# Optimization experiments

Hardware: AMD Instinct MI355X
Metric: run time of the kernel (lower is better)

## Reference

```python
import jax, jax.numpy as jnp
import numpy as np

B, C, D, DE, NH = 4, 4, 96, 96, 3
NS, HIN, TOTAL_Z, PZ = 12, 128, 64, 32
WZ = WH = WW = 4
N_WIN_TOK = WZ * WH * WW  # 64 tokens per 3D window


def _rel_index():
    # standard Swin-3D relative position index, (N, N) into a (7*7*7, NH) table
    c = np.stack(np.meshgrid(np.arange(WZ), np.arange(WH), np.arange(WW), indexing='ij')).reshape(3, -1)
    r = (c[:, :, None] - c[:, None, :]).transpose(1, 2, 0)
    r += np.array([WZ - 1, WH - 1, WW - 1])
    r[:, :, 0] *= (2 * WH - 1) * (2 * WW - 1)
    r[:, :, 1] *= (2 * WW - 1)
    return jnp.asarray(r.sum(-1))

REL_IDX = _rel_index()


def layernorm(x, g, b, eps=1e-5):
    m = x.mean(-1, keepdims=True)
    v = x.var(-1, keepdims=True)
    return (x - m) * jax.lax.rsqrt(v + eps) * g + b


def groupnorm(x, g, b, groups=8, eps=1e-5):
    Bb, Cc, Z, H, W = x.shape
    xr = x.reshape(Bb, groups, Cc // groups, Z, H, W)
    m = xr.mean((2, 3, 4, 5), keepdims=True)
    v = xr.var((2, 3, 4, 5), keepdims=True)
    xr = (xr - m) * jax.lax.rsqrt(v + eps)
    return xr.reshape(Bb, Cc, Z, H, W) * g[None, :, None, None, None] + b[None, :, None, None, None]


def conv3d(x, w, b):
    y = jax.lax.conv_general_dilated(x, w, (1, 1, 1), 'SAME', dimension_numbers=('NCDHW', 'OIDHW', 'NCDHW'))
    return y + b[None, :, None, None, None]


def z_interp(x, pos, out_z):
    """Linear interp along z. x:(B,C,S,H,W), pos:(S,) sorted float positions.
    Matches the torch loop: clamp below first / above last, weight=0.5 on ties."""
    S = x.shape[2]
    zq = jnp.arange(out_z, dtype=jnp.float32)
    right = jnp.searchsorted(pos, zq, side='left')  # first i with pos[i] >= z
    left = jnp.clip(right - 1, 0, S - 1)
    rc = jnp.clip(right, 0, S - 1)
    lp, rp = pos[left], pos[rc]
    d = rp - lp
    w = jnp.where(d > 0, (zq - lp) / jnp.where(d > 0, d, 1.0), 0.5)
    w = w[None, None, :, None, None]
    return (1.0 - w) * x[:, :, left] + w * x[:, :, rc]


def reference(sparse_obs, encoder_feat, pe_w, pe_b, pe_g, pe_beta, enc_w, enc_b, ln_g, ln_b,
              qkv_w, qkv_b, attn_w, attn_b, rpb, ref_w1, ref_b1, gn1_g, gn1_b,
              ref_w2, ref_b2, gn2_g, gn2_b, rec_w, rec_b, sparse_indices):
    Bb, Cc, Sz, H, W = sparse_obs.shape
    pos = sparse_indices.astype(jnp.float32)
    # --- skip connection: z-interp baseline at full resolution ---
    baseline = z_interp(sparse_obs, pos, TOTAL_Z)  # (B,C,64,128,128)
    # --- sparse patch embed: conv (1,4,4) stride (1,4,4) + LN ---
    xr = sparse_obs.reshape(Bb, Cc, Sz, H // 4, 4, W // 4, 4)
    f = jnp.einsum('bczhpwq,dcpq->bdzhw', xr, pe_w) + pe_b[None, :, None, None, None]
    f = layernorm(f.transpose(0, 2, 3, 4, 1), pe_g, pe_beta).transpose(0, 4, 1, 2, 3)
    # position-aware z interpolation into patch space (patch_size_z = 2)
    f = z_interp(f, pos / 2.0, PZ)  # (B,D,32,32,32)
    # --- encoder 1x1x1 projection + fuse ---
    enc = jnp.einsum('bczhw,dc->bdzhw', encoder_feat, enc_w) + enc_b[None, :, None, None, None]
    f = f + enc
    # --- 3D window attention with relative position bias (pre-norm, residual) ---
    nz = PZ // WZ
    x = f.transpose(0, 2, 3, 4, 1)  # (B,Z,H,W,D)
    xw = x.reshape(Bb, nz, WZ, nz, WH, nz, WW, D).transpose(0, 1, 3, 5, 2, 4, 6, 7).reshape(-1, N_WIN_TOK, D)
    sc = xw
    xn = layernorm(xw, ln_g, ln_b)
    dh = D // NH
    qkv = (xn @ qkv_w.T + qkv_b).reshape(-1, N_WIN_TOK, 3, NH, dh).transpose(2, 0, 3, 1, 4)
    q, k, v = qkv[0], qkv[1], qkv[2]  # (nWin*B, NH, N, dh)
    att = jnp.einsum('whnd,whmd->whnm', q * (dh ** -0.5), k)
    att = att + rpb[REL_IDX].transpose(2, 0, 1)[None]  # (.., NH, N, N)
    att = jax.nn.softmax(att, axis=-1)
    o = jnp.einsum('whnm,whmd->whnd', att, v).transpose(0, 2, 1, 3).reshape(-1, N_WIN_TOK, D)
    xw = sc + (o @ attn_w.T + attn_b)
    x = xw.reshape(Bb, nz, nz, nz, WZ, WH, WW, D).transpose(0, 1, 4, 2, 5, 3, 6, 7).reshape(Bb, PZ, PZ, PZ, D)
    f = x.transpose(0, 4, 1, 2, 3)
    f = jax.nn.gelu(groupnorm(conv3d(f, ref_w1, ref_b1), gn1_g, gn1_b), approximate=False)
    f = jax.nn.gelu(groupnorm(conv3d(f, ref_w2, ref_b2), gn2_g, gn2_b), approximate=False)
    # --- patch recovery: ConvTranspose3d kernel=stride=(2,4,4) as einsum+reshape ---
    delta = jnp.einsum('bizhw,iodef->bozdhewf', f, rec_w).reshape(Bb, Cc, PZ * 2, PZ * 4, PZ * 4)
    delta = delta + rec_b[None, :, None, None, None]
    return baseline + delta


def setup_inputs():
    key = jax.random.key(0)
    ks = jax.random.split(key, 16)
    n = lambda i, shape: jax.random.normal(ks[i], shape, dtype=jnp.float32) * 0.02
    return {
        'sparse_obs': jax.random.normal(ks[0], (B, C, NS, HIN, HIN), dtype=jnp.float32),
        'encoder_feat': jax.random.normal(ks[1], (B, DE, PZ, PZ, PZ), dtype=jnp.float32),
        'pe_w': n(2, (D, C, 4, 4)), 'pe_b': jnp.zeros((D,)), 'pe_g': jnp.ones((D,)), 'pe_beta': jnp.zeros((D,)),
        'enc_w': n(3, (D, DE)), 'enc_b': jnp.zeros((D,)),
        'ln_g': jnp.ones((D,)), 'ln_b': jnp.zeros((D,)),
        'qkv_w': n(4, (3 * D, D)), 'qkv_b': jnp.zeros((3 * D,)),
        'attn_w': n(5, (D, D)), 'attn_b': jnp.zeros((D,)),
        'rpb': n(6, ((2 * WZ - 1) * (2 * WH - 1) * (2 * WW - 1), NH)),
        'ref_w1': n(7, (D, D, 3, 3, 3)), 'ref_b1': jnp.zeros((D,)), 'gn1_g': jnp.ones((D,)), 'gn1_b': jnp.zeros((D,)),
        'ref_w2': n(8, (D, D, 3, 3, 3)), 'ref_b2': jnp.zeros((D,)), 'gn2_g': jnp.ones((D,)), 'gn2_b': jnp.zeros((D,)),
        'rec_w': n(9, (D, C, 2, 4, 4)), 'rec_b': jnp.zeros((C,)),
        'sparse_indices': jnp.asarray(np.round(np.linspace(0, 63, 12)).astype(np.int64)),
    }
```

## Files before the change

kernel.cpp:

```cpp
#include <hip/hip_runtime.h>
#include <math.h>

typedef __attribute__((ext_vector_type(8))) short short8v;
typedef __attribute__((ext_vector_type(4))) float float4v;

__device__ inline unsigned short f2bf(float f) {
  unsigned u = __float_as_uint(f);
  return (unsigned short)((u + 0x7fff + ((u >> 16) & 1)) >> 16);
}
__device__ inline unsigned pk2(float a, float b) {
  return (unsigned)f2bf(a) | ((unsigned)f2bf(b) << 16);
}
__device__ inline float bfl(unsigned u) { return __uint_as_float(u << 16); }
__device__ inline float bfh(unsigned u) { return __uint_as_float(u & 0xffff0000u); }
__device__ inline float bfs(short s) { return __uint_as_float(((unsigned)(unsigned short)s) << 16); }

__global__ __launch_bounds__(96) void k_tables(const int* __restrict__ sidx, int* __restrict__ T) {
  __shared__ float pos[12];
  int t = threadIdx.x;
  if (t < 12) pos[t] = (float)sidx[t];
  __syncthreads();
  if (t < 64) {
    float zq = (float)t;
    int r = 0;
    while (r < 12 && pos[r] < zq) r++;
    int l = r - 1; if (l < 0) l = 0; if (l > 11) l = 11;
    int rc = r; if (rc > 11) rc = 11;
    float lp = pos[l], rp = pos[rc], d = rp - lp;
    float w = d > 0.f ? (zq - lp) / d : 0.5f;
    T[t] = l; T[64 + t] = rc; ((float*)T)[128 + t] = w;
  } else {
    int zq = t - 64;
    float zqf = (float)zq;
    int r = 0;
    while (r < 12 && pos[r] * 0.5f < zqf) r++;
    int l = r - 1; if (l < 0) l = 0; if (l > 11) l = 11;
    int rc = r; if (rc > 11) rc = 11;
    float lp = pos[l] * 0.5f, rp = pos[rc] * 0.5f, d = rp - lp;
    float w = d > 0.f ? (zqf - lp) / d : 0.5f;
    T[192 + zq] = l; T[224 + zq] = rc; ((float*)T)[256 + zq] = w;
  }
}

__global__ __launch_bounds__(256) void k_wcv(const float* __restrict__ w, short* __restrict__ Wt) {
  int id = blockIdx.x * 256 + threadIdx.x;
  if (id >= 248832) return;
  float v = w[id];
  int o = id / 2592; int rem = id % 2592; int i = rem / 27; int tap = rem % 27;
  Wt[(tap * 96 + o) * 96 + i] = (short)f2bf(v);
}

__global__ __launch_bounds__(256) void k_cvt(const float* __restrict__ src, short* __restrict__ dst, int n) {
  int id = blockIdx.x * 256 + threadIdx.x;
  if (id < n) dst[id] = (short)f2bf(src[id]);
}

__global__ __launch_bounds__(256) void k_wrt(const float* __restrict__ src, short* __restrict__ dst) {
  int id = blockIdx.x * 256 + threadIdx.x;
  if (id >= 12288) return;
  int i = id >> 7, j = id & 127;
  dst[j * 96 + i] = (short)f2bf(src[id]);
}

__global__ __launch_bounds__(256) void k_bias(const float* __restrict__ rpb, float* __restrict__ Bt) {
  int id = blockIdx.x * 256 + threadIdx.x;
  if (id >= 12288) return;
  int head = id >> 12, rem = id & 4095, n = rem >> 6, m = rem & 63;
  int dz = (n >> 4) - (m >> 4), dh = ((n >> 2) & 3) - ((m >> 2) & 3), dw = (n & 3) - (m & 3);
  Bt[id] = rpb[((dz + 3) * 49 + (dh + 3) * 7 + (dw + 3)) * 3 + head];
}

__global__ __launch_bounds__(256) void k_pe(const float* __restrict__ sp, const short* __restrict__ Wpe,
    const float* __restrict__ pb, const float* __restrict__ pg, const float* __restrict__ pbeta,
    float* __restrict__ f1) {
  int x = blockIdx.x;
  int b = x / 384, z = (x / 32) % 12, h = x % 32;
  __shared__ short sB[32][72];
  __shared__ float sF[32][97];
  __shared__ float sM[32], sR[32];
  int tid = threadIdx.x;
  for (int id = tid; id < 2048; id += 256) {
    int c = id >> 9, p = (id >> 7) & 3, col = id & 127;
    float v = sp[(((b * 4 + c) * 12 + z) * 128 + h * 4 + p) * 128 + col];
    sB[col >> 2][c * 16 + p * 4 + (col & 3)] = (short)f2bf(v);
  }
  __syncthreads();
  int w = tid >> 6, l = tid & 63, lo = l & 15, ig = l >> 4;
  int nt = w & 1, mbase = (w >> 1) * 3;
  short8v bfrag[2];
  #pragma unroll
  for (int kc = 0; kc < 2; kc++)
    bfrag[kc] = *(const short8v*)&sB[nt * 16 + lo][kc * 32 + ig * 8];
  #pragma unroll
  for (int mi = 0; mi < 3; mi++) {
    int m = mbase + mi;
    float4v acc = (float4v){0.f, 0.f, 0.f, 0.f};
    #pragma unroll
    for (int kc = 0; kc < 2; kc++) {
      short8v a = *(const short8v*)(Wpe + (size_t)(m * 16 + lo) * 64 + kc * 32 + ig * 8);
      acc = __builtin_amdgcn_mfma_f32_16x16x32_bf16(a, bfrag[kc], acc, 0, 0, 0);
    }
    int wcoord = nt * 16 + lo;
    #pragma unroll
    for (int r = 0; r < 4; r++) {
      int d = m * 16 + ig * 4 + r;
      sF[wcoord][d] = acc[r] + pb[d];
    }
  }
  __syncthreads();
  if (tid < 32) {
    int wv = tid;
    float s = 0.f, ss = 0.f;
    for (int d = 0; d < 96; d++) { float v = sF[wv][d]; s += v; ss += v * v; }
    float m = s * (1.f / 96.f);
    float var = ss * (1.f / 96.f) - m * m;
    sM[wv] = m; sR[wv] = rsqrtf(var + 1e-5f);
  }
  __syncthreads();
  for (int id = tid; id < 3072; id += 256) {
    int d = id >> 5, wv = id & 31;
    float v = (sF[wv][d] - sM[wv]) * sR[wv] * pg[d] + pbeta[d];
    f1[(((b * 96 + d) * 12 + z) * 32 + h) * 32 + wv] = v;
  }
}

__global__ __launch_bounds__(256) void k_ie(const float* __restrict__ f1, const float* __restrict__ ef,
    const short* __restrict__ Wenc, const float* __restrict__ eb, const int* __restrict__ T,
    unsigned* __restrict__ Xg) {
  int x = blockIdx.x;
  int b = x >> 9, chunk = x & 511;
  int v0 = chunk * 64;
  int z = v0 >> 10, rp = v0 & 1023;
  int zl = T[192 + z], zr = T[224 + z];
  float wt = ((const float*)T)[256 + z];
  __shared__ short sEb[64][104];
  int tid = threadIdx.x;
  for (int id = tid; id < 6144; id += 256) {
    int c = id >> 6, vs = id & 63;
    sEb[vs][c] = (short)f2bf(ef[(size_t)(b * 96 + c) * 32768 + v0 + vs]);
  }
  __syncthreads();
  int w = tid >> 6, l = tid & 63, lo = l & 15, ig = l >> 4;
  int vcol = w * 16 + lo;
  short8v bfrag[3];
  #pragma unroll
  for (int kc = 0; kc < 3; kc++)
    bfrag[kc] = *(const short8v*)&sEb[vcol][kc * 32 + ig * 8];
  float4v acc[6];
  #pragma unroll
  for (int m = 0; m < 6; m++) {
    acc[m] = (float4v){0.f, 0.f, 0.f, 0.f};
    #pragma unroll
    for (int kc = 0; kc < 3; kc++) {
      short8v a = *(const short8v*)(Wenc + (size_t)(m * 16 + lo) * 96 + kc * 32 + ig * 8);
      acc[m] = __builtin_amdgcn_mfma_f32_16x16x32_bf16(a, bfrag[kc], acc[m], 0, 0, 0);
    }
  }
  int zb = z >> 2, tz = z & 3;
  int h0 = (chunk & 15) * 2;
  int h = h0 + (vcol >> 5), wc = vcol & 31;
  int win = ((b * 8 + zb) * 8 + (h >> 2)) * 8 + (wc >> 2);
  int t = tz * 16 + (h & 3) * 4 + (wc & 3);
  size_t xbase = (size_t)(win * 64 + t) * 48;
  float wl = 1.f - wt;
  #pragma unroll
  for (int m = 0; m < 6; m++) {
    #pragma unroll
    for (int rr = 0; rr < 2; rr++) {
      int d0 = m * 16 + ig * 4 + rr * 2;
      const float* p1a = f1 + ((size_t)(b * 96 + d0) * 12 + zl) * 1024 + rp + vcol;
      const float* p2a = f1 + ((size_t)(b * 96 + d0) * 12 + zr) * 1024 + rp + vcol;
      const float* p1b = f1 + ((size_t)(b * 96 + d0 + 1) * 12 + zl) * 1024 + rp + vcol;
      const float* p2b = f1 + ((size_t)(b * 96 + d0 + 1) * 12 + zr) * 1024 + rp + vcol;
      float va = acc[m][rr * 2] + eb[d0] + wl * p1a[0] + wt * p2a[0];
      float vb = acc[m][rr * 2 + 1] + eb[d0 + 1] + wl * p1b[0] + wt * p2b[0];
      Xg[xbase + m * 8 + ig * 2 + rr] = pk2(va, vb);
    }
  }
}

__global__ __launch_bounds__(512) void k_qkv(const unsigned* __restrict__ Xg, const short* __restrict__ Wq,
    const float* __restrict__ qb, const float* __restrict__ lg, const float* __restrict__ lb,
    short* __restrict__ Qg, short* __restrict__ Kg, short* __restrict__ Vg) {
  int win = blockIdx.x;
  __shared__ short sX[64][104];
  __shared__ short sVt[96][72];
  __shared__ float sM[64], sRr[64];
  int tid = threadIdx.x;
  for (int id = tid; id < 3072; id += 512) {
    int row = id / 48, c2 = id % 48;
    *(unsigned*)&sX[row][c2 * 2] = Xg[(size_t)(win * 64 + row) * 48 + c2];
  }
  __syncthreads();
  {
    int token = tid >> 3, j = tid & 7;
    float s = 0.f, ss = 0.f;
    #pragma unroll
    for (int i = 0; i < 12; i++) {
      float v = bfs(sX[token][j * 12 + i]);
      s += v; ss += v * v;
    }
    s += __shfl_xor(s, 1); ss += __shfl_xor(ss, 1);
    s += __shfl_xor(s, 2); ss += __shfl_xor(ss, 2);
    s += __shfl_xor(s, 4); ss += __shfl_xor(ss, 4);
    if (j == 0) {
      float m = s * (1.f / 96.f);
      sM[token] = m;
      sRr[token] = rsqrtf(ss * (1.f / 96.f) - m * m + 1e-5f);
    }
  }
  __syncthreads();
  for (int id = tid; id < 3072; id += 512) {
    int row = id / 48, c2 = id % 48;
    unsigned u = *(unsigned*)&sX[row][c2 * 2];
    float m = sM[row], r = sRr[row];
    float v0 = (bfl(u) - m) * r * lg[2 * c2] + lb[2 * c2];
    float v1 = (bfh(u) - m) * r * lg[2 * c2 + 1] + lb[2 * c2 + 1];
    *(unsigned*)&sX[row][c2 * 2] = pk2(v0, v1);
  }
  __syncthreads();
  int w = tid >> 6, l = tid & 63, lo = l & 15, ig = l >> 4;
  int mt2 = w >> 1, nh = w & 1;
  short8v a[3];
  #pragma unroll
  for (int kc = 0; kc < 3; kc++)
    a[kc] = *(const short8v*)&sX[mt2 * 16 + lo][kc * 32 + ig * 8];
  for (int nt = nh * 9; nt < nh * 9 + 9; nt++) {
    float4v acc = (float4v){0.f, 0.f, 0.f, 0.f};
    #pragma unroll
    for (int kc = 0; kc < 3; kc++) {
      short8v bfr = *(const short8v*)(Wq + (size_t)(nt * 16 + lo) * 96 + kc * 32 + ig * 8);
      acc = __builtin_amdgcn_mfma_f32_16x16x32_bf16(a[kc], bfr, acc, 0, 0, 0);
    }
    int out = nt * 16 + lo;
    float bias = qb[out];
    if (nt < 6) {
      int head = out >> 5, c = out & 31;
      #pragma unroll
      for (int r = 0; r < 4; r++)
        Qg[((size_t)(win * 3 + head) * 64 + mt2 * 16 + ig * 4 + r) * 32 + c] =
            (short)f2bf((acc[r] + bias) * 0.17677669529663687f);
    } else if (nt < 12) {
      int o2 = out - 96, head = o2 >> 5, c = o2 & 31;
      #pragma unroll
      for (int r = 0; r < 4; r++)
        Kg[((size_t)(win * 3 + head) * 64 + mt2 * 16 + ig * 4 + r) * 32 + c] = (short)f2bf(acc[r] + bias);
    } else {
      int o2 = out - 192;
      #pragma unroll
      for (int r = 0; r < 4; r++)
        sVt[o2][mt2 * 16 + ig * 4 + r] = (short)f2bf(acc[r] + bias);
    }
  }
  __syncthreads();
  for (int id = tid; id < 768; id += 512) {
    int row = id >> 3, ch = id & 7;
    short8v v = *(short8v*)&sVt[row][ch * 8];
    *(short8v*)(Vg + ((size_t)(win * 3 + (row >> 5)) * 32 + (row & 31)) * 64 + ch * 8) = v;
  }
}

__global__ __launch_bounds__(256) void k_att2(const short* __restrict__ Qg, const short* __restrict__ Kg,
    const short* __restrict__ Vg, const float* __restrict__ Bt, short* __restrict__ Og) {
  __shared__ short Pl[4][64][72];
  int tid = threadIdx.x;
  int w = tid >> 6, l = tid & 63, lo = l & 15, ig = l >> 4;
  int gwh = blockIdx.x * 4 + w;
  int head = gwh % 3, win = gwh / 3;
  short8v q[4], k[4];
  #pragma unroll
  for (int mt = 0; mt < 4; mt++)
    q[mt] = *(const short8v*)(Qg + ((size_t)gwh * 64 + mt * 16 + lo) * 32 + ig * 8);
  #pragma unroll
  for (int nt = 0; nt < 4; nt++)
    k[nt] = *(const short8v*)(Kg + ((size_t)gwh * 64 + nt * 16 + lo) * 32 + ig * 8);
  float4v s[4][4];
  #pragma unroll
  for (int mt = 0; mt < 4; mt++)
    #pragma unroll
    for (int nt = 0; nt < 4; nt++)
      s[mt][nt] = __builtin_amdgcn_mfma_f32_16x16x32_bf16(q[mt], k[nt], (float4v){0.f, 0.f, 0.f, 0.f}, 0, 0, 0);
  const float* bt = Bt + head * 4096;
  #pragma unroll
  for (int mt = 0; mt < 4; mt++) {
    #pragma unroll
    for (int r = 0; r < 4; r++) {
      int tok = mt * 16 + ig * 4 + r;
      float v[4];
      float mx = -1e30f;
      #pragma unroll
      for (int nt = 0; nt < 4; nt++) {
        v[nt] = s[mt][nt][r] + bt[tok * 64 + nt * 16 + lo];
        mx = fmaxf(mx, v[nt]);
      }
      mx = fmaxf(mx, __shfl_xor(mx, 1));
      mx = fmaxf(mx, __shfl_xor(mx, 2));
      mx = fmaxf(mx, __shfl_xor(mx, 4));
      mx = fmaxf(mx, __shfl_xor(mx, 8));
      float sm = 0.f;
      #pragma unroll
      for (int nt = 0; nt < 4; nt++) { v[nt] = __expf(v[nt] - mx); sm += v[nt]; }
      sm += __shfl_xor(sm, 1);
      sm += __shfl_xor(sm, 2);
      sm += __shfl_xor(sm, 4);
      sm += __shfl_xor(sm, 8);
      float inv = 1.f / sm;
      #pragma unroll
      for (int nt = 0; nt < 4; nt++)
        Pl[w][tok][nt * 16 + lo] = (short)f2bf(v[nt] * inv);
    }
  }
  short8v pa[4][2], vb[2][2];
  #pragma unroll
  for (int mt = 0; mt < 4; mt++)
    #pragma unroll
    for (int kc = 0; kc < 2; kc++)
      pa[mt][kc] = *(const short8v*)&Pl[w][mt * 16 + lo][kc * 32 + ig * 8];
  #pragma unroll
  for (int ct = 0; ct < 2; ct++)
    #pragma unroll
    for (int kc = 0; kc < 2; kc++)
      vb[ct][kc] = *(const short8v*)(Vg + ((size_t)gwh * 32 + ct * 16 + lo) * 64 + kc * 32 + ig * 8);
  #pragma unroll
  for (int mt = 0; mt < 4; mt++)
    #pragma unroll
    for (int ct = 0; ct < 2; ct++) {
      float4v o = __builtin_amdgcn_mfma_f32_16x16x32_bf16(pa[mt][0], vb[ct][0], (float4v){0.f, 0.f, 0.f, 0.f}, 0, 0, 0);
      o = __builtin_amdgcn_mfma_f32_16x16x32_bf16(pa[mt][1], vb[ct][1], o, 0, 0, 0);
      #pragma unroll
      for (int r = 0; r < 4; r++)
        Og[((size_t)(win * 64 + mt * 16 + ig * 4 + r)) * 96 + head * 32 + ct * 16 + lo] = (short)f2bf(o[r]);
    }
}

__global__ __launch_bounds__(256) void k_proj(const short* __restrict__ Og, const unsigned* __restrict__ Xg,
    const short* __restrict__ Wa, const float* __restrict__ ab, short* __restrict__ Xt) {
  int win = blockIdx.x;
  __shared__ float sOut[64][100];
  int tid = threadIdx.x;
  int w = tid >> 6, l = tid & 63, lo = l & 15, ig = l >> 4;
  int mt = w;
  short8v a[3];
  #pragma unroll
  for (int kc = 0; kc < 3; kc++)
    a[kc] = *(const short8v*)(Og + ((size_t)(win * 64 + mt * 16 + lo)) * 96 + kc * 32 + ig * 8);
  #pragma unroll
  for (int nt = 0; nt < 6; nt++) {
    float4v acc = (float4v){0.f, 0.f, 0.f, 0.f};
    #pragma unroll
    for (int kc = 0; kc < 3; kc++) {
      short8v bfr = *(const short8v*)(Wa + (size_t)(nt * 16 + lo) * 96 + kc * 32 + ig * 8);
      acc = __builtin_amdgcn_mfma_f32_16x16x32_bf16(a[kc], bfr, acc, 0, 0, 0);
    }
    int out = nt * 16 + lo;
    float bias = ab[out];
    #pragma unroll
    for (int r = 0; r < 4; r++) {
      int tok = mt * 16 + ig * 4 + r;
      unsigned u = Xg[(size_t)(win * 64 + tok) * 48 + (out >> 1)];
      sOut[tok][out] = acc[r] + bias + ((out & 1) ? bfh(u) : bfl(u));
    }
  }
  __syncthreads();
  int b = win >> 9, zb = (win >> 6) & 7, hb = (win >> 3) & 7, wb = win & 7;
  for (int id = tid; id < 3072; id += 256) {
    int cc = id >> 10, rem = id & 1023, t = rem >> 4, ilp = rem & 15;
    int d0 = cc * 32 + ilp * 2;
    unsigned pk = pk2(sOut[t][d0], sOut[t][d0 + 1]);
    int tz = t >> 4, th = (t >> 2) & 3, tw = t & 3;
    size_t vox = (size_t)(zb * 4 + tz) * 1024 + (hb * 4 + th) * 32 + wb * 4 + tw;
    ((unsigned*)Xt)[((size_t)(b * 3 + cc) * 32768 + vox) * 16 + ilp] = pk;
  }
}

__global__ __launch_bounds__(256) void k_convM(const short* __restrict__ Xt,
    const short* __restrict__ Wt, const float* __restrict__ cb, short* __restrict__ y16,
    float* __restrict__ stats) {
  int x = blockIdx.x;
  int b = x >> 7, zp = (x >> 3) & 15, hq = x & 7;
  int tid = threadIdx.x;
  int wvi = tid >> 6, l = tid & 63;
  int lo = l & 15, ig = l >> 4;
  int hp = wvi & 1, mh = wvi >> 1;
  __shared__ short Xl[816 * 32];
  __shared__ float sG[16];
  if (tid < 16) sG[tid] = 0.f;
  float4v acc[3][2][2][2];
  #pragma unroll
  for (int mi = 0; mi < 3; mi++)
    #pragma unroll
    for (int zo = 0; zo < 2; zo++)
      #pragma unroll
      for (int hr = 0; hr < 2; hr++)
        #pragma unroll
        for (int n = 0; n < 2; n++) acc[mi][zo][hr][n] = (float4v){0.f, 0.f, 0.f, 0.f};

  for (int c = 0; c < 3; c++) {
    __syncthreads();
    for (int r = 0; r < 13; r++) {
      int id = tid + 256 * r;
      if (id < 3264) {
        int seg = id & 3, q = id >> 2;
        int zz = q / 204, rem = q - zz * 204;
        int hh = rem / 34, ww = rem - hh * 34;
        int gz = zp * 2 + zz - 1, gh = hq * 4 + hh - 1, gw = ww - 1;
        int4 val = {0, 0, 0, 0};
        if (gz >= 0 && gz < 32 && gh >= 0 && gh < 32 && gw >= 0 && gw < 32)
          val = *(const int4*)(Xt + ((size_t)((b * 3 + c) * 32768 + (gz << 10) + (gh << 5) + gw) * 32 + seg * 8));
        int slot = seg ^ ((q >> 1) & 3);
        *(int4*)(&Xl[q * 32 + slot * 8]) = val;
      }
    }
    __syncthreads();
    for (int dh = 0; dh < 3; dh++) {
      for (int dwv = 0; dwv < 3; dwv++) {
        short8v bfr[4][2][2];
        #pragma unroll
        for (int zr = 0; zr < 4; zr++)
          #pragma unroll
          for (int hr = 0; hr < 2; hr++)
            #pragma unroll
            for (int n = 0; n < 2; n++) {
              int vox = (zr * 6 + hp * 2 + hr + dh) * 34 + n * 16 + lo + dwv;
              bfr[zr][hr][n] = *(const short8v*)&Xl[vox * 32 + ((ig ^ ((vox >> 1) & 3)) * 8)];
            }
        #pragma unroll
        for (int dz = 0; dz < 3; dz++) {
          int tap = dz * 9 + dh * 3 + dwv;
          #pragma unroll
          for (int mi = 0; mi < 3; mi++) {
            short8v wf = *(const short8v*)(Wt +
                ((size_t)(tap * 96 + (mh * 3 + mi) * 16 + lo)) * 96 + c * 32 + ig * 8);
            #pragma unroll
            for (int zo = 0; zo < 2; zo++)
              #pragma unroll
              for (int hr = 0; hr < 2; hr++)
                #pragma unroll
                for (int n = 0; n < 2; n++)
                  acc[mi][zo][hr][n] = __builtin_amdgcn_mfma_f32_16x16x32_bf16(wf, bfr[zo + dz][hr][n], acc[mi][zo][hr][n], 0, 0, 0);
          }
        }
      }
    }
  }
  #pragma unroll
  for (int mi = 0; mi < 3; mi++) {
    #pragma unroll
    for (int r = 0; r < 4; r++) {
      int o = (mh * 3 + mi) * 16 + ig * 4 + r;
      float cbo = cb[o];
      float s = 0.f, ss = 0.f;
      #pragma unroll
      for (int zo = 0; zo < 2; zo++)
        #pragma unroll
        for (int hr = 0; hr < 2; hr++)
          #pragma unroll
          for (int n = 0; n < 2; n++) {
            float v = acc[mi][zo][hr][n][r] + cbo;
            int z = zp * 2 + zo;
            int h = hq * 4 + hp * 2 + hr;
            int vcol = n * 16 + lo;
            y16[((size_t)(b * 96 + o) << 15) + (z << 10) + (h << 5) + vcol] = (short)f2bf(v);
            s += v; ss += v * v;
          }
      s += __shfl_xor(s, 1); ss += __shfl_xor(ss, 1);
      s += __shfl_xor(s, 2); ss += __shfl_xor(ss, 2);
      s += __shfl_xor(s, 4); ss += __shfl_xor(ss, 4);
      s += __shfl_xor(s, 8); ss += __shfl_xor(ss, 8);
      if (lo == 0) {
        int gl = o / 12;
        atomicAdd(&sG[gl * 2], s);
        atomicAdd(&sG[gl * 2 + 1], ss);
      }
    }
  }
  __syncthreads();
  if (tid < 16) atomicAdd(&stats[b * 16 + tid], sG[tid]);
}

__global__ __launch_bounds__(256) void k_gn(const short* __restrict__ y16, const float* __restrict__ stats,
    const float* __restrict__ gg, const float* __restrict__ gb, short* __restrict__ xt) {
  int x = blockIdx.x;
  int b = x / 1536, r = x % 1536, c = r / 512, vt = r % 512;
  int v0 = vt * 64;
  __shared__ float sT[64][33];
  int tid = threadIdx.x;
  const float invN = 1.f / 393216.f;
  {
    int ol = tid >> 3, vq = tid & 7;
    int o = c * 32 + ol, g = b * 8 + o / 12;
    float m = stats[2 * g] * invN;
    float var = stats[2 * g + 1] * invN - m * m;
    float rs = rsqrtf(var + 1e-5f) * gg[o];
    float bb = gb[o];
    short8v yv = *(const short8v*)&y16[((size_t)(b * 96 + o) << 15) + v0 + vq * 8];
    #pragma unroll
    for (int j = 0; j < 8; j++) {
      float val = (bfs(yv[j]) - m) * rs + bb;
      sT[vq * 8 + j][ol] = 0.5f * val * (1.f + erff(val * 0.70710678118654752f));
    }
  }
  __syncthreads();
  for (int id = tid; id < 1024; id += 256) {
    int v = id >> 4, p = id & 15;
    ((unsigned*)xt)[((size_t)(b * 3 + c) * 32768 + v0 + v) * 16 + p] = pk2(sT[v][2 * p], sT[v][2 * p + 1]);
  }
}

__global__ __launch_bounds__(256) void k_final(const short* __restrict__ f5b, const float* __restrict__ sp,
    const short* __restrict__ Wrec, const float* __restrict__ rb, const int* __restrict__ T,
    float* __restrict__ out) {
  int x = blockIdx.x;
  int b = x >> 10, chunk = x & 1023;
  int z = chunk >> 5, h = chunk & 31;
  int v0 = chunk * 32;
  int tid = threadIdx.x;
  int w = tid >> 6, l = tid & 63, lo = l & 15, ig = l >> 4;
  short8v afrag[2][3];
  #pragma unroll
  for (int mt = 0; mt < 2; mt++)
    #pragma unroll
    for (int kc = 0; kc < 3; kc++)
      afrag[mt][kc] = *(const short8v*)(f5b +
          ((size_t)(b * 3 + kc) * 32768 + v0 + mt * 16 + lo) * 32 + ig * 8);
  float4v acc[2][2];
  #pragma unroll
  for (int nt2 = 0; nt2 < 2; nt2++) {
    int jt = w * 2 + nt2;
    #pragma unroll
    for (int mt = 0; mt < 2; mt++) acc[mt][nt2] = (float4v){0.f, 0.f, 0.f, 0.f};
    #pragma unroll
    for (int kc = 0; kc < 3; kc++) {
      short8v bfr = *(const short8v*)(Wrec + (size_t)(jt * 16 + lo) * 96 + kc * 32 + ig * 8);
      #pragma unroll
      for (int mt = 0; mt < 2; mt++)
        acc[mt][nt2] = __builtin_amdgcn_mfma_f32_16x16x32_bf16(afrag[mt][kc], bfr, acc[mt][nt2], 0, 0, 0);
    }
  }
  const float* w64 = (const float*)(T + 128);
  #pragma unroll
  for (int mt = 0; mt < 2; mt++)
    #pragma unroll
    for (int nt2 = 0; nt2 < 2; nt2++) {
      int jt = w * 2 + nt2;
      #pragma unroll
      for (int r = 0; r < 4; r++) {
        int wv = mt * 16 + ig * 4 + r;
        int j = jt * 16 + lo;
        int o = j >> 5, dd = (j >> 4) & 1, e = (j >> 2) & 3, ff = j & 3;
        int Z = 2 * z + dd, H = 4 * h + e, W = 4 * wv + ff;
        int zl = T[Z], zr = T[64 + Z];
        float bw = w64[Z];
        const float* spb = sp + (size_t)(b * 4 + o) * 196608;
        float bval = (1.f - bw) * spb[(size_t)zl * 16384 + H * 128 + W]
                   + bw * spb[(size_t)zr * 16384 + H * 128 + W];
        out[((size_t)(b * 4 + o) * 64 + Z) * 16384 + H * 128 + W] = bval + acc[mt][nt2][r] + rb[o];
      }
    }
}

extern "C" void kernel_launch(void* const* d_in, const int* in_sizes, int n_in,
                              void* d_out, int out_size, void* d_ws, size_t ws_size,
                              hipStream_t stream) {
  const float* sp    = (const float*)d_in[0];
  const float* ef    = (const float*)d_in[1];
  const float* pe_w  = (const float*)d_in[2];
  const float* pe_b  = (const float*)d_in[3];
  const float* pe_g  = (const float*)d_in[4];
  const float* pe_be = (const float*)d_in[5];
  const float* enc_w = (const float*)d_in[6];
  const float* enc_b = (const float*)d_in[7];
  const float* ln_g  = (const float*)d_in[8];
  const float* ln_b  = (const float*)d_in[9];
  const float* qkv_w = (const float*)d_in[10];
  const float* qkv_b = (const float*)d_in[11];
  const float* at_w  = (const float*)d_in[12];
  const float* at_b  = (const float*)d_in[13];
  const float* rpb   = (const float*)d_in[14];
  const float* w1    = (const float*)d_in[15];
  const float* b1    = (const float*)d_in[16];
  const float* g1g   = (const float*)d_in[17];
  const float* g1b   = (const float*)d_in[18];
  const float* w2    = (const float*)d_in[19];
  const float* b2    = (const float*)d_in[20];
  const float* g2g   = (const float*)d_in[21];
  const float* g2b   = (const float*)d_in[22];
  const float* recw  = (const float*)d_in[23];
  const float* recb  = (const float*)d_in[24];
  const int*   sidx  = (const int*)d_in[25];
  float* out = (float*)d_out;

  char* ws = (char*)d_ws;
  unsigned* Xg = (unsigned*)ws;
  float* f1    = (float*)(ws + 25165824);
  short* Qg    = (short*)(ws + 25165824);
  short* Kg    = (short*)(ws + 50331648);
  short* Vg    = (short*)(ws + 75497472);
  short* XtA   = (short*)(ws + 25165824);
  short* Y16   = (short*)(ws + 50331648);
  int*   T     = (int*)(ws + 100663296);
  float* stats = (float*)(ws + 100665344);
  short* Wrec  = (short*)(ws + 100666368);

  char* dob = (char*)d_out;
  short* Og   = (short*)d_out;
  short* Wenc = (short*)(dob + 25165824);
  short* Wpe  = (short*)(dob + 25184256);
  short* Wqkv = (short*)(dob + 65937408);
  short* Waw  = (short*)(dob + 65992704);
  float* Bt   = (float*)(dob + 66011136);
  short* Wt1  = (short*)(dob + 66060288);
  short* Wt2  = (short*)(dob + 66557952);

  k_tables<<<1, 96, 0, stream>>>(sidx, T);
  k_wcv<<<972, 256, 0, stream>>>(w1, Wt1);
  k_wcv<<<972, 256, 0, stream>>>(w2, Wt2);
  k_cvt<<<108, 256, 0, stream>>>(qkv_w, Wqkv, 27648);
  k_cvt<<<36, 256, 0, stream>>>(at_w, Waw, 9216);
  k_cvt<<<36, 256, 0, stream>>>(enc_w, Wenc, 9216);
  k_cvt<<<24, 256, 0, stream>>>(pe_w, Wpe, 6144);
  k_wrt<<<48, 256, 0, stream>>>(recw, Wrec);
  k_bias<<<48, 256, 0, stream>>>(rpb, Bt);

  k_pe<<<1536, 256, 0, stream>>>(sp, Wpe, pe_b, pe_g, pe_be, f1);
  k_ie<<<2048, 256, 0, stream>>>(f1, ef, Wenc, enc_b, T, Xg);
  k_qkv<<<2048, 512, 0, stream>>>(Xg, Wqkv, qkv_b, ln_g, ln_b, Qg, Kg, Vg);
  k_att2<<<1536, 256, 0, stream>>>(Qg, Kg, Vg, Bt, Og);
  k_proj<<<2048, 256, 0, stream>>>(Og, Xg, Waw, at_b, XtA);

  hipMemsetAsync(stats, 0, 64 * sizeof(float), stream);
  k_convM<<<512, 256, 0, stream>>>(XtA, Wt1, b1, Y16, stats);
  k_gn<<<6144, 256, 0, stream>>>(Y16, stats, g1g, g1b, XtA);

  hipMemsetAsync(stats, 0, 64 * sizeof(float), stream);
  k_convM<<<512, 256, 0, stream>>>(XtA, Wt2, b2, Y16, stats);
  k_gn<<<6144, 256, 0, stream>>>(Y16, stats, g2g, g2b, XtA);

  k_final<<<4096, 256, 0, stream>>>(XtA, sp, Wrec, recb, T, out);
}
```

Baseline: 357.4 us.

## Fuse QKV, window attention and output projection into one per-window kernel

Merges k_qkv, k_att2 and k_proj into a single kernel, k_fatt, with one block per window. Q, K, V, the softmax probabilities and the attention output now stay in shared memory. This removes three launches and the global round-trips of Q/K/V and the attention output. In exchange, the block drops to 256 threads, each wave handles all three heads one after another, and shared memory use per block rises, which may lower occupancy.

```diff
diff --git a/kernel.cpp b/kernel.cpp
--- a/kernel.cpp
+++ b/kernel.cpp
@@ -179,118 +179,109 @@
   }
 }
 
-__global__ __launch_bounds__(512) void k_qkv(const unsigned* __restrict__ Xg, const short* __restrict__ Wq,
-    const float* __restrict__ qb, const float* __restrict__ lg, const float* __restrict__ lb,
-    short* __restrict__ Qg, short* __restrict__ Kg, short* __restrict__ Vg) {
+__global__ __launch_bounds__(256) void k_fatt(const unsigned* __restrict__ Xg,
+    const short* __restrict__ Wq, const float* __restrict__ qb,
+    const float* __restrict__ lg, const float* __restrict__ lb,
+    const short* __restrict__ Wa, const float* __restrict__ ab,
+    const float* __restrict__ Bt, short* __restrict__ Xt) {
   int win = blockIdx.x;
-  __shared__ short sX[64][104];
-  __shared__ short sVt[96][72];
-  __shared__ float sM[64], sRr[64];
+  __shared__ short sA[64][104];
+  __shared__ short sN[64][104];
+  __shared__ short sK[192][40];
+  __shared__ short sVt[96][88];
+  __shared__ short sQP[4][16][104];
+  __shared__ float sMn[64], sRs[64];
   int tid = threadIdx.x;
-  for (int id = tid; id < 3072; id += 512) {
+  int w = tid >> 6, l = tid & 63, lo = l & 15, ig = l >> 4;
+  const float scale = 0.17677669529663687f;
+
+  for (int id = tid; id < 3072; id += 256) {
     int row = id / 48, c2 = id % 48;
-    *(unsigned*)&sX[row][c2 * 2] = Xg[(size_t)(win * 64 + row) * 48 + c2];
+    *(unsigned*)&sA[row][c2 * 2] = Xg[(size_t)(win * 64 + row) * 48 + c2];
   }
   __syncthreads();
   {
-    int token = tid >> 3, j = tid & 7;
+    int token = tid >> 2, jl = tid & 3;
     float s = 0.f, ss = 0.f;
     #pragma unroll
     for (int i = 0; i < 12; i++) {
-      float v = bfs(sX[token][j * 12 + i]);
-      s += v; ss += v * v;
+      unsigned u = *(unsigned*)&sA[token][jl * 24 + i * 2];
+      float v0 = bfl(u), v1 = bfh(u);
+      s += v0 + v1; ss += v0 * v0 + v1 * v1;
     }
     s += __shfl_xor(s, 1); ss += __shfl_xor(ss, 1);
     s += __shfl_xor(s, 2); ss += __shfl_xor(ss, 2);
-    s += __shfl_xor(s, 4); ss += __shfl_xor(ss, 4);
-    if (j == 0) {
+    if (jl == 0) {
       float m = s * (1.f / 96.f);
-      sM[token] = m;
-      sRr[token] = rsqrtf(ss * (1.f / 96.f) - m * m + 1e-5f);
-    }
-  }
-  __syncthreads();
-  for (int id = tid; id < 3072; id += 512) {
+      sMn[token] = m;
+      sRs[token] = rsqrtf(ss * (1.f / 96.f) - m * m + 1e-5f);
+    }
+  }
+  __syncthreads();
+  for (int id = tid; id < 3072; id += 256) {
     int row = id / 48, c2 = id % 48;
-    unsigned u = *(unsigned*)&sX[row][c2 * 2];
-    float m = sM[row], r = sRr[row];
+    unsigned u = *(unsigned*)&sA[row][c2 * 2];
+    float m = sMn[row], r = sRs[row];
     float v0 = (bfl(u) - m) * r * lg[2 * c2] + lb[2 * c2];
     float v1 = (bfh(u) - m) * r * lg[2 * c2 + 1] + lb[2 * c2 + 1];
-    *(unsigned*)&sX[row][c2 * 2] = pk2(v0, v1);
-  }
-  __syncthreads();
-  int w = tid >> 6, l = tid & 63, lo = l & 15, ig = l >> 4;
-  int mt2 = w >> 1, nh = w & 1;
-  short8v a[3];
-  #pragma unroll
-  for (int kc = 0; kc < 3; kc++)
-    a[kc] = *(const short8v*)&sX[mt2 * 16 + lo][kc * 32 + ig * 8];
-  for (int nt = nh * 9; nt < nh * 9 + 9; nt++) {
-    float4v acc = (float4v){0.f, 0.f, 0.f, 0.f};
-    #pragma unroll
-    for (int kc = 0; kc < 3; kc++) {
-      short8v bfr = *(const short8v*)(Wq + (size_t)(nt * 16 + lo) * 96 + kc * 32 + ig * 8);
-      acc = __builtin_amdgcn_mfma_f32_16x16x32_bf16(a[kc], bfr, acc, 0, 0, 0);
-    }
-    int out = nt * 16 + lo;
-    float bias = qb[out];
-    if (nt < 6) {
-      int head = out >> 5, c = out & 31;
-      #pragma unroll
-      for (int r = 0; r < 4; r++)
-        Qg[((size_t)(win * 3 + head) * 64 + mt2 * 16 + ig * 4 + r) * 32 + c] =
-            (short)f2bf((acc[r] + bias) * 0.17677669529663687f);
-    } else if (nt < 12) {
-      int o2 = out - 96, head = o2 >> 5, c = o2 & 31;
-      #pragma unroll
-      for (int r = 0; r < 4; r++)
-        Kg[((size_t)(win * 3 + head) * 64 + mt2 * 16 + ig * 4 + r) * 32 + c] = (short)f2bf(acc[r] + bias);
-    } else {
-      int o2 = out - 192;
-      #pragma unroll
-      for (int r = 0; r < 4; r++)
-        sVt[o2][mt2 * 16 + ig * 4 + r] = (short)f2bf(acc[r] + bias);
-    }
-  }
-  __syncthreads();
-  for (int id = tid; id < 768; id += 512) {
-    int row = id >> 3, ch = id & 7;
-    short8v v = *(short8v*)&sVt[row][ch * 8];
-    *(short8v*)(Vg + ((size_t)(win * 3 + (row >> 5)) * 32 + (row & 31)) * 64 + ch * 8) = v;
-  }
-}
-
-__global__ __launch_bounds__(256) void k_att2(const short* __restrict__ Qg, const short* __restrict__ Kg,
-    const short* __restrict__ Vg, const float* __restrict__ Bt, short* __restrict__ Og) {
-  __shared__ short Pl[4][64][72];
-  int tid = threadIdx.x;
-  int w = tid >> 6, l = tid & 63, lo = l & 15, ig = l >> 4;
-  int gwh = blockIdx.x * 4 + w;
-  int head = gwh % 3, win = gwh / 3;
-  short8v q[4], k[4];
-  #pragma unroll
-  for (int mt = 0; mt < 4; mt++)
-    q[mt] = *(const short8v*)(Qg + ((size_t)gwh * 64 + mt * 16 + lo) * 32 + ig * 8);
-  #pragma unroll
-  for (int nt = 0; nt < 4; nt++)
-    k[nt] = *(const short8v*)(Kg + ((size_t)gwh * 64 + nt * 16 + lo) * 32 + ig * 8);
-  float4v s[4][4];
-  #pragma unroll
-  for (int mt = 0; mt < 4; mt++)
+    *(unsigned*)&sN[row][c2 * 2] = pk2(v0, v1);
+  }
+  __syncthreads();
+  {
+    short8v a[3];
+    #pragma unroll
+    for (int kc = 0; kc < 3; kc++)
+      a[kc] = *(const short8v*)&sN[w * 16 + lo][kc * 32 + ig * 8];
+    for (int nt = 0; nt < 18; nt++) {
+      float4v acc = (float4v){0.f, 0.f, 0.f, 0.f};
+      #pragma unroll
+      for (int kc = 0; kc < 3; kc++) {
+        short8v bfr = *(const short8v*)(Wq + (size_t)(nt * 16 + lo) * 96 + kc * 32 + ig * 8);
+        acc = __builtin_amdgcn_mfma_f32_16x16x32_bf16(a[kc], bfr, acc, 0, 0, 0);
+      }
+      int out = nt * 16 + lo;
+      float bias = qb[out];
+      if (nt < 6) {
+        int head = out >> 5, c = out & 31;
+        #pragma unroll
+        for (int r = 0; r < 4; r++)
+          sQP[w][ig * 4 + r][head * 32 + c] = (short)f2bf((acc[r] + bias) * scale);
+      } else if (nt < 12) {
+        int o2 = out - 96, head = o2 >> 5, c = o2 & 31;
+        #pragma unroll
+        for (int r = 0; r < 4; r++)
+          sK[head * 64 + w * 16 + ig * 4 + r][c] = (short)f2bf(acc[r] + bias);
+      } else {
+        int o2 = out - 192;
+        #pragma unroll
+        for (int r = 0; r < 4; r++)
+          sVt[o2][w * 16 + ig * 4 + r] = (short)f2bf(acc[r] + bias);
+      }
+    }
+  }
+  __syncthreads();
+  short8v qf[3];
+  #pragma unroll
+  for (int h = 0; h < 3; h++)
+    qf[h] = *(const short8v*)&sQP[w][lo][h * 32 + ig * 8];
+  for (int h = 0; h < 3; h++) {
+    short8v kf[4];
     #pragma unroll
     for (int nt = 0; nt < 4; nt++)
-      s[mt][nt] = __builtin_amdgcn_mfma_f32_16x16x32_bf16(q[mt], k[nt], (float4v){0.f, 0.f, 0.f, 0.f}, 0, 0, 0);
-  const float* bt = Bt + head * 4096;
-  #pragma unroll
-  for (int mt = 0; mt < 4; mt++) {
+      kf[nt] = *(const short8v*)&sK[h * 64 + nt * 16 + lo][ig * 8];
+    float4v s[4];
+    #pragma unroll
+    for (int nt = 0; nt < 4; nt++)
+      s[nt] = __builtin_amdgcn_mfma_f32_16x16x32_bf16(qf[h], kf[nt], (float4v){0.f, 0.f, 0.f, 0.f}, 0, 0, 0);
+    const float* bt = Bt + h * 4096;
     #pragma unroll
     for (int r = 0; r < 4; r++) {
-      int tok = mt * 16 + ig * 4 + r;
+      int tok = w * 16 + ig * 4 + r;
       float v[4];
       float mx = -1e30f;
       #pragma unroll
       for (int nt = 0; nt < 4; nt++) {
-        v[nt] = s[mt][nt][r] + bt[tok * 64 + nt * 16 + lo];
+        v[nt] = s[nt][r] + bt[tok * 64 + nt * 16 + lo];
         mx = fmaxf(mx, v[nt]);
       }
       mx = fmaxf(mx, __shfl_xor(mx, 1));
@@ -307,66 +298,52 @@
       float inv = 1.f / sm;
       #pragma unroll
       for (int nt = 0; nt < 4; nt++)
-        Pl[w][tok][nt * 16 + lo] = (short)f2bf(v[nt] * inv);
-    }
-  }
-  short8v pa[4][2], vb[2][2];
-  #pragma unroll
-  for (int mt = 0; mt < 4; mt++)
+        sQP[w][ig * 4 + r][nt * 16 + lo] = (short)f2bf(v[nt] * inv);
+    }
+    short8v pa[2];
     #pragma unroll
     for (int kc = 0; kc < 2; kc++)
-      pa[mt][kc] = *(const short8v*)&Pl[w][mt * 16 + lo][kc * 32 + ig * 8];
-  #pragma unroll
-  for (int ct = 0; ct < 2; ct++)
-    #pragma unroll
-    for (int kc = 0; kc < 2; kc++)
-      vb[ct][kc] = *(const short8v*)(Vg + ((size_t)gwh * 32 + ct * 16 + lo) * 64 + kc * 32 + ig * 8);
-  #pragma unroll
-  for (int mt = 0; mt < 4; mt++)
+      pa[kc] = *(const short8v*)&sQP[w][lo][kc * 32 + ig * 8];
     #pragma unroll
     for (int ct = 0; ct < 2; ct++) {
-      float4v o = __builtin_amdgcn_mfma_f32_16x16x32_bf16(pa[mt][0], vb[ct][0], (float4v){0.f, 0.f, 0.f, 0.f}, 0, 0, 0);
-      o = __builtin_amdgcn_mfma_f32_16x16x32_bf16(pa[mt][1], vb[ct][1], o, 0, 0, 0);
+      short8v vb0 = *(const short8v*)&sVt[h * 32 + ct * 16 + lo][ig * 8];
+      short8v vb1 = *(const short8v*)&sVt[h * 32 + ct * 16 + lo][32 + ig * 8];
+      float4v o = __builtin_amdgcn_mfma_f32_16x16x32_bf16(pa[0], vb0, (float4v){0.f, 0.f, 0.f, 0.f}, 0, 0, 0);
+      o = __builtin_amdgcn_mfma_f32_16x16x32_bf16(pa[1], vb1, o, 0, 0, 0);
       #pragma unroll
       for (int r = 0; r < 4; r++)
-        Og[((size_t)(win * 64 + mt * 16 + ig * 4 + r)) * 96 + head * 32 + ct * 16 + lo] = (short)f2bf(o[r]);
-    }
-}
-
-__global__ __launch_bounds__(256) void k_proj(const short* __restrict__ Og, const unsigned* __restrict__ Xg,
-    const short* __restrict__ Wa, const float* __restrict__ ab, short* __restrict__ Xt) {
-  int win = blockIdx.x;
-  __shared__ float sOut[64][100];
-  int tid = threadIdx.x;
-  int w = tid >> 6, l = tid & 63, lo = l & 15, ig = l >> 4;
-  int mt = w;
-  short8v a[3];
-  #pragma unroll
-  for (int kc = 0; kc < 3; kc++)
-    a[kc] = *(const short8v*)(Og + ((size_t)(win * 64 + mt * 16 + lo)) * 96 + kc * 32 + ig * 8);
-  #pragma unroll
-  for (int nt = 0; nt < 6; nt++) {
-    float4v acc = (float4v){0.f, 0.f, 0.f, 0.f};
-    #pragma unroll
-    for (int kc = 0; kc < 3; kc++) {
-      short8v bfr = *(const short8v*)(Wa + (size_t)(nt * 16 + lo) * 96 + kc * 32 + ig * 8);
-      acc = __builtin_amdgcn_mfma_f32_16x16x32_bf16(a[kc], bfr, acc, 0, 0, 0);
-    }
-    int out = nt * 16 + lo;
-    float bias = ab[out];
-    #pragma unroll
-    for (int r = 0; r < 4; r++) {
-      int tok = mt * 16 + ig * 4 + r;
-      unsigned u = Xg[(size_t)(win * 64 + tok) * 48 + (out >> 1)];
-      sOut[tok][out] = acc[r] + bias + ((out & 1) ? bfh(u) : bfl(u));
+        sA[w * 16 + ig * 4 + r][h * 32 + ct * 16 + lo] = (short)f2bf(o[r]);
+    }
+  }
+  {
+    short8v a[3];
+    #pragma unroll
+    for (int kc = 0; kc < 3; kc++)
+      a[kc] = *(const short8v*)&sA[w * 16 + lo][kc * 32 + ig * 8];
+    #pragma unroll
+    for (int nt = 0; nt < 6; nt++) {
+      float4v acc = (float4v){0.f, 0.f, 0.f, 0.f};
+      #pragma unroll
+      for (int kc = 0; kc < 3; kc++) {
+        short8v bfr = *(const short8v*)(Wa + (size_t)(nt * 16 + lo) * 96 + kc * 32 + ig * 8);
+        acc = __builtin_amdgcn_mfma_f32_16x16x32_bf16(a[kc], bfr, acc, 0, 0, 0);
+      }
+      int out = nt * 16 + lo;
+      float bias = ab[out];
+      #pragma unroll
+      for (int r = 0; r < 4; r++) {
+        int tok = w * 16 + ig * 4 + r;
+        unsigned u = Xg[(size_t)(win * 64 + tok) * 48 + (out >> 1)];
+        float res = (out & 1) ? bfh(u) : bfl(u);
+        sN[tok][out] = (short)f2bf(acc[r] + bias + res);
+      }
     }
   }
   __syncthreads();
   int b = win >> 9, zb = (win >> 6) & 7, hb = (win >> 3) & 7, wb = win & 7;
   for (int id = tid; id < 3072; id += 256) {
     int cc = id >> 10, rem = id & 1023, t = rem >> 4, ilp = rem & 15;
-    int d0 = cc * 32 + ilp * 2;
-    unsigned pk = pk2(sOut[t][d0], sOut[t][d0 + 1]);
+    unsigned pk = *(unsigned*)&sN[t][cc * 32 + ilp * 2];
     int tz = t >> 4, th = (t >> 2) & 3, tw = t & 3;
     size_t vox = (size_t)(zb * 4 + tz) * 1024 + (hb * 4 + th) * 32 + wb * 4 + tw;
     ((unsigned*)Xt)[((size_t)(b * 3 + cc) * 32768 + vox) * 16 + ilp] = pk;
@@ -593,9 +570,6 @@
   char* ws = (char*)d_ws;
   unsigned* Xg = (unsigned*)ws;
   float* f1    = (float*)(ws + 25165824);
-  short* Qg    = (short*)(ws + 25165824);
-  short* Kg    = (short*)(ws + 50331648);
-  short* Vg    = (short*)(ws + 75497472);
   short* XtA   = (short*)(ws + 25165824);
   short* Y16   = (short*)(ws + 50331648);
   int*   T     = (int*)(ws + 100663296);
@@ -603,7 +577,6 @@
   short* Wrec  = (short*)(ws + 100666368);
 
   char* dob = (char*)d_out;
-  short* Og   = (short*)d_out;
   short* Wenc = (short*)(dob + 25165824);
   short* Wpe  = (short*)(dob + 25184256);
   short* Wqkv = (short*)(dob + 65937408);
@@ -624,9 +597,7 @@
 
   k_pe<<<1536, 256, 0, stream>>>(sp, Wpe, pe_b, pe_g, pe_be, f1);
   k_ie<<<2048, 256, 0, stream>>>(f1, ef, Wenc, enc_b, T, Xg);
-  k_qkv<<<2048, 512, 0, stream>>>(Xg, Wqkv, qkv_b, ln_g, ln_b, Qg, Kg, Vg);
-  k_att2<<<1536, 256, 0, stream>>>(Qg, Kg, Vg, Bt, Og);
-  k_proj<<<2048, 256, 0, stream>>>(Og, Xg, Waw, at_b, XtA);
+  k_fatt<<<2048, 256, 0, stream>>>(Xg, Wqkv, qkv_b, ln_g, ln_b, Waw, at_b, Bt, XtA);
 
   hipMemsetAsync(stats, 0, 64 * sizeof(float), stream);
   k_convM<<<512, 256, 0, stream>>>(XtA, Wt1, b1, Y16, stats);
```

After: 359.9 us. About the same (+0.7%).
